# Kernel optimization log

Measured on AMD Instinct MI355X. Metric: run time of the kernel, lower is better.

## Reference

```python
import jax, jax.numpy as jnp
import numpy as np

KS = 5               # kernel_size per spline dimension
K3 = KS ** 3         # 125 weight matrices per SplineConv
NS = [16384, 4096, 1024, 256, 64]  # nodes per hierarchy level
DEG = 8


def spline_basis(pseudo):
    """Degree-1 open B-spline basis for 3D pseudo-coords in [0,1].
    Returns basis [E,8] and weight indices [E,8] into the K3 weights."""
    v = pseudo * (KS - 1)
    bot = jnp.minimum(jnp.floor(v), KS - 2)
    frac = v - bot                                  # [E,3]
    bot = bot.astype(jnp.int32)
    bits = jnp.array([[(s >> d) & 1 for d in range(3)] for s in range(8)], jnp.int32)  # [8,3]
    f = frac[:, None, :]                            # [E,1,3]
    basis = jnp.prod(jnp.where(bits[None] == 1, f, 1.0 - f), axis=-1)   # [E,8]
    strides = jnp.array([1, KS, KS * KS], jnp.int32)
    widx = jnp.sum((bot[:, None, :] + bits[None]) * strides, axis=-1)   # [E,8]
    return basis, widx


def spline_conv(x, src, dst, basis, widx, W, root, bias, n):
    """out_j = (1/deg_j) * sum_{i->j} sum_s B_s(u_ij) x_i W_{k(s)} + x_j root + bias.
    Accumulate basis-weighted source features into per-(node, weight-index)
    buckets, then one dense einsum with the 125 kernel weights."""
    in_c = x.shape[1]
    contrib = basis[..., None] * x[src][:, None, :]          # [E,8,in]
    flat = (dst[:, None] * K3 + widx).reshape(-1)            # [E*8]
    acc = jnp.zeros((n * K3, in_c), x.dtype).at[flat].add(contrib.reshape(-1, in_c))
    out = jnp.einsum('nki,kio->no', acc.reshape(n, K3, in_c), W)
    deg = jnp.zeros((n,), x.dtype).at[dst].add(1.0)
    return out / jnp.maximum(deg, 1.0)[:, None] + x @ root + bias


def setup_inputs() -> dict:
    rng = np.random.default_rng(0)
    inp = {}
    inp['x'] = jnp.asarray(rng.standard_normal((NS[0], 1)), jnp.float32)
    for l in range(4):
        e = NS[l] * DEG
        inp[f'src{l}'] = jnp.asarray(rng.integers(0, NS[l], e), jnp.int32)
        inp[f'dst{l}'] = jnp.asarray(rng.integers(0, NS[l], e), jnp.int32)
        inp[f'pseudo{l}'] = jnp.asarray(rng.random((e, 3)), jnp.float32)
        cl = np.arange(NS[l]) % NS[l + 1]  # guarantees every voxel cluster non-empty
        rng.shuffle(cl)
        inp[f'cluster{l}'] = jnp.asarray(cl, jnp.int32)
    chans = [(1, 32), (32, 32), (32, 64), (64, 64), (64, 64), (64, 64), (64, 64), (64, 64)]
    names = ['1', '12', '2', '3', '4', '5', '6', '7']
    for nm, (ci, co) in zip(names, chans):
        inp[f'W{nm}'] = jnp.asarray(rng.standard_normal((K3, ci, co)) / np.sqrt(8.0 * ci), jnp.float32)
        inp[f'R{nm}'] = jnp.asarray(rng.standard_normal((ci, co)) / np.sqrt(ci), jnp.float32)
        inp[f'B{nm}'] = jnp.zeros((co,), jnp.float32)
    inp['fc1_w'] = jnp.asarray(rng.standard_normal((64, 64)) / 8.0, jnp.float32)
    inp['fc1_b'] = jnp.zeros((64,), jnp.float32)
    inp['fc2_w'] = jnp.asarray(rng.standard_normal((64, 10)) / 8.0, jnp.float32)
    inp['fc2_b'] = jnp.zeros((10,), jnp.float32)
    return inp


def reference(x, pseudo0, pseudo1, pseudo2, pseudo3,
              src0, dst0, src1, dst1, src2, dst2, src3, dst3,
              cluster0, cluster1, cluster2, cluster3,
              W1, R1, B1, W12, R12, B12, W2, R2, B2, W3, R3, B3,
              W4, R4, B4, W5, R5, B5, W6, R6, B6, W7, R7, B7,
              fc1_w, fc1_b, fc2_w, fc2_b):
    elu = jax.nn.elu
    # level 0
    b, wi = spline_basis(pseudo0)
    h = elu(spline_conv(x, src0, dst0, b, wi, W1, R1, B1, NS[0]))
    h = elu(spline_conv(h, src0, dst0, b, wi, W12, R12, B12, NS[0]))
    h = jax.ops.segment_max(h, cluster0, num_segments=NS[1])   # voxel max pool 1
    # level 1
    b, wi = spline_basis(pseudo1)
    h = elu(spline_conv(h, src1, dst1, b, wi, W2, R2, B2, NS[1]))
    h = elu(spline_conv(h, src1, dst1, b, wi, W3, R3, B3, NS[1]))
    h = jax.ops.segment_max(h, cluster1, num_segments=NS[2])   # voxel max pool 2
    # level 2
    b, wi = spline_basis(pseudo2)
    h = elu(spline_conv(h, src2, dst2, b, wi, W4, R4, B4, NS[2]))
    h = elu(spline_conv(h, src2, dst2, b, wi, W5, R5, B5, NS[2]))
    h = jax.ops.segment_max(h, cluster2, num_segments=NS[3])   # voxel max pool 3
    # level 3
    b, wi = spline_basis(pseudo3)
    h = elu(spline_conv(h, src3, dst3, b, wi, W6, R6, B6, NS[3]))
    h = elu(spline_conv(h, src3, dst3, b, wi, W7, R7, B7, NS[3]))
    h = jax.ops.segment_max(h, cluster3, num_segments=NS[4])   # voxel max pool 4
    # readout head (dropout is identity in eval mode)
    g = h.mean(0)[None, :]
    g = g @ fc1_w + fc1_b
    g = g @ fc2_w + fc2_b
    return jax.nn.log_softmax(g, axis=1)
```

## Files before the change

kernel.cpp:

```cpp
#include <hip/hip_runtime.h>
#include <hip/hip_bf16.h>

#define KS 5
#define K3 125

typedef __attribute__((ext_vector_type(8))) short short8;
typedef __attribute__((ext_vector_type(4))) float floatx4;

__device__ inline unsigned enc_f(float f) {
    int b = __float_as_int(f);
    return (b >= 0) ? ((unsigned)b | 0x80000000u) : ~((unsigned)b);
}

__device__ inline unsigned short f2bf(float f) {
    unsigned u = __float_as_uint(f);
    u += 0x7FFFu + ((u >> 16) & 1u);
    return (unsigned short)(u >> 16);
}
__device__ inline float bf2f(unsigned short h) {
    return __uint_as_float((unsigned)h << 16);
}
__device__ inline unsigned pack2bf(float a, float b) {
    return (unsigned)f2bf(a) | ((unsigned)f2bf(b) << 16);
}

__device__ inline void edge_basis(const float* __restrict__ pseudo, int e,
                                  float* bs, int* ks) {
    float fr[3];
    int bot[3];
#pragma unroll
    for (int d = 0; d < 3; ++d) {
        float v = pseudo[e * 3 + d] * (float)(KS - 1);
        float fl = fminf(floorf(v), (float)(KS - 2));
        fr[d] = v - fl;
        bot[d] = (int)fl;
    }
    const int strides[3] = {1, KS, KS * KS};
#pragma unroll
    for (int s = 0; s < 8; ++s) {
        float b = 1.f;
        int w = 0;
#pragma unroll
        for (int d = 0; d < 3; ++d) {
            int bit = (s >> d) & 1;
            b *= bit ? fr[d] : (1.f - fr[d]);
            w += (bot[d] + bit) * strides[d];
        }
        bs[s] = b;
        ks[s] = w;
    }
}

__device__ inline void edge_fracs(const float* __restrict__ pseudo, int e, float* bs) {
    float fr[3];
#pragma unroll
    for (int d = 0; d < 3; ++d) {
        float v = pseudo[e * 3 + d] * (float)(KS - 1);
        float fl = fminf(floorf(v), (float)(KS - 2));
        fr[d] = v - fl;
    }
#pragma unroll
    for (int s = 0; s < 8; ++s) {
        float b = 1.f;
#pragma unroll
        for (int d = 0; d < 3; ++d) b *= ((s >> d) & 1) ? fr[d] : (1.f - fr[d]);
        bs[s] = b;
    }
}

__device__ inline int edge_bucket(const float* __restrict__ pseudo, int e) {
    int kb = 0;
#pragma unroll
    for (int d = 0; d < 3; ++d) {
        float v = pseudo[e * 3 + d] * (float)(KS - 1);
        int fl = (int)fminf(floorf(v), (float)(KS - 2));
        kb += fl << (2 * d);
    }
    return kb;
}

__global__ __launch_bounds__(256) void pre1(
    const float* __restrict__ p0, const float* __restrict__ p1,
    const float* __restrict__ p2, const float* __restrict__ p3,
    const int* __restrict__ d0, const int* __restrict__ d1,
    const int* __restrict__ d2, const int* __restrict__ d3,
    const int* __restrict__ c0, const int* __restrict__ c1,
    const int* __restrict__ c2, const int* __restrict__ c3,
    const float* __restrict__ w12, const float* __restrict__ w2,
    const float* __restrict__ w3, const float* __restrict__ w4,
    const float* __restrict__ w5, const float* __restrict__ w6,
    const float* __restrict__ w7,
    int* __restrict__ hpart, int* __restrict__ degi,
    int* __restrict__ ccnt, int* __restrict__ clist,
    short* __restrict__ Wt, int* __restrict__ posArr) {
    __shared__ float wls[64 * 65];
    __shared__ int h[64];
    int b = blockIdx.x;
    int t = threadIdx.x;
    if (b >= 765) {
        int sl = b - 765;
        const float* srcp;
        int IC, OC, lgI, lgO, per;
        size_t obase;
        if (sl < 125) {
            IC = 32; OC = 32; lgI = 5; lgO = 5; per = 1024;
            srcp = w12 + (size_t)sl * 1024;
            obase = (size_t)sl * 1024;
        } else if (sl < 250) {
            int k = sl - 125;
            IC = 32; OC = 64; lgI = 5; lgO = 6; per = 2048;
            srcp = w2 + (size_t)k * 2048;
            obase = 128000 + (size_t)k * 2048;
        } else {
            int q = sl - 250;
            int ts = q / 125;
            int k = q - ts * 125;
            const float* Ws[5] = {w3, w4, w5, w6, w7};
            IC = 64; OC = 64; lgI = 6; lgO = 6; per = 4096;
            srcp = Ws[ts] + (size_t)k * 4096;
            obase = 384000 + (size_t)ts * 512000 + (size_t)k * 4096;
        }
        for (int r = t; r < per; r += 256) {
            int i = r >> lgO, o = r & (OC - 1);
            wls[i * (OC + 1) + o] = srcp[r];
        }
        __syncthreads();
        for (int j = t; j < per; j += 256) {
            int o = j >> lgI, i = j & (IC - 1);
            Wt[obase + j] = (short)f2bf(wls[i * (OC + 1) + o]);
        }
        return;
    }
    if (b >= 680) {
        int idx = (b - 680) * 256 + t;
        int j, cof, nof;
        const int* cl;
        if (idx < 16384)      { j = idx;         cl = c0; cof = 0;    nof = 0; }
        else if (idx < 20480) { j = idx - 16384; cl = c1; cof = 4096; nof = 16384; }
        else if (idx < 21504) { j = idx - 20480; cl = c2; cof = 5120; nof = 20480; }
        else if (idx < 21760) { j = idx - 21504; cl = c3; cof = 5376; nof = 21504; }
        else return;
        int c = cl[j];
        int slot = atomicAdd(&ccnt[cof + c], 1) & 3;
        clist[nof + c * 4 + slot] = j;
        return;
    }
    int l, lb, E, dof, eof_;
    const float* ps;
    const int* ds;
    if (b < 512)      { l = 0; lb = b;       ps = p0; ds = d0; E = 131072; dof = 0;     eof_ = 0; }
    else if (b < 640) { l = 1; lb = b - 512; ps = p1; ds = d1; E = 32768;  dof = 16384; eof_ = 131072; }
    else if (b < 672) { l = 2; lb = b - 640; ps = p2; ds = d2; E = 8192;   dof = 20480; eof_ = 163840; }
    else              { l = 3; lb = b - 672; ps = p3; ds = d3; E = 2048;   dof = 21504; eof_ = 172032; }
    if (t < 64) h[t] = 0;
    __syncthreads();
    int e = lb * 256 + t;
    if (e < E) {
        atomicAdd(&h[edge_bucket(ps, e)], 1);
        int rel = atomicAdd(&degi[dof + ds[e]], 1);
        posArr[eof_ + e] = rel;
    }
    __syncthreads();
    if (t < 64) hpart[b * 64 + t] = h[t];
}

__global__ __launch_bounds__(1024) void pre2(const int* __restrict__ hpart,
                                             int* __restrict__ bbase,
                                             int* __restrict__ tileOf,
                                             int* __restrict__ pack,
                                             const int* __restrict__ degi,
                                             int* __restrict__ off) {
    int b = blockIdx.x;
    int t = threadIdx.x;
    __shared__ int ls[1024];
    __shared__ int aux[192];
    if (b < 4) {
        const int Nv[4] = {16384, 4096, 1024, 256};
        const int DOFv[4] = {0, 16384, 20480, 21504};
        const int OFFv[4] = {0, 16385, 20482, 21507};
        int l = b;
        int n = Nv[l];
        const int* d = degi + DOFv[l];
        int* o = off + OFFv[l];
        int per = (n + 1023) >> 10;
        int beg = t * per;
        int end = (beg + per < n) ? beg + per : n;
        int s = 0;
        for (int j = beg; j < end; ++j) s += d[j];
        ls[t] = s;
        __syncthreads();
        for (int dd = 1; dd < 1024; dd <<= 1) {
            int v = (t >= dd) ? ls[t - dd] : 0;
            __syncthreads();
            ls[t] += v;
            __syncthreads();
        }
        int base = (t == 0) ? 0 : ls[t - 1];
        for (int j = beg; j < end; ++j) {
            o[j] = base;
            base += d[j];
        }
        if (t == 1023) o[n] = ls[1023];
    } else {
        const int TBv[4] = {0, 2112, 2688, 2880};
        const int MTv[4] = {2112, 576, 192, 96};
        const int HBv[4] = {0, 512, 640, 672};
        const int NBv[4] = {512, 128, 32, 8};
        int l = b - 4;
        int tileBase = TBv[l];
        int hb = HBv[l], nb = NBv[l];
        int bucket = t & 63, seg = t >> 6;
        int rps = (nb + 15) >> 4;
        int r0 = seg * rps;
        int r1 = r0 + rps;
        if (r1 > nb) r1 = nb;
        int ssum = 0;
        for (int lb = r0; lb < r1; ++lb) ssum += hpart[(hb + lb) * 64 + bucket];
        ls[seg * 64 + bucket] = ssum;
        __syncthreads();
        int pre = 0;
        for (int s2 = 0; s2 < seg; ++s2) pre += ls[s2 * 64 + bucket];
        if (seg == 15) aux[bucket] = pre + ssum;
        __syncthreads();
        if (t < 64) aux[64 + t] = (aux[t] + 63) >> 6;
        __syncthreads();
        for (int d = 1; d < 64; d <<= 1) {
            int v = 0;
            if (t < 64 && t >= d) v = aux[64 + t - d];
            __syncthreads();
            if (t < 64) aux[64 + t] += v;
            __syncthreads();
        }
        if (t < 64) {
            int cnt = aux[t];
            int tiles = (cnt + 63) >> 6;
            int tb = tileBase + aux[64 + t] - tiles;
            int gstart = tb * 64;
            aux[128 + t] = gstart;
            for (int q = 0; q < tiles; ++q) tileOf[tb + q] = t;
            for (int idx = gstart + cnt; idx < (tb + tiles) * 64; ++idx) pack[idx] = -1;
            if (t == 63) {
                for (int q = tileBase + aux[64 + 63]; q < tileBase + MTv[l]; ++q)
                    tileOf[q] = -1;
            }
        }
        __syncthreads();
        int run = aux[128 + bucket] + pre;
        for (int lb = r0; lb < r1; ++lb) {
            bbase[(hb + lb) * 64 + bucket] = run;
            run += hpart[(hb + lb) * 64 + bucket];
        }
    }
}

__global__ __launch_bounds__(256) void scatter_pos_all(
    const float* __restrict__ p0, const float* __restrict__ p1,
    const float* __restrict__ p2, const float* __restrict__ p3,
    const int* __restrict__ d0, const int* __restrict__ d1,
    const int* __restrict__ d2, const int* __restrict__ d3,
    const int* __restrict__ bbase, const int* __restrict__ csr,
    int* __restrict__ pack, int* __restrict__ posArr,
    int* __restrict__ esrt) {
    int b = blockIdx.x;
    int l, lb, E, eof_, cof;
    const float* ps;
    const int* ds;
    if (b < 512)      { l = 0; lb = b;       ps = p0; ds = d0; E = 131072; eof_ = 0;      cof = 0; }
    else if (b < 640) { l = 1; lb = b - 512; ps = p1; ds = d1; E = 32768;  eof_ = 131072; cof = 16385; }
    else if (b < 672) { l = 2; lb = b - 640; ps = p2; ds = d2; E = 8192;   eof_ = 163840; cof = 20482; }
    else              { l = 3; lb = b - 672; ps = p3; ds = d3; E = 2048;   eof_ = 172032; cof = 21507; }
    const int* csrL = csr + cof;
    __shared__ int h[64], lbk[64], gb[64], sh[64];
    __shared__ int sp[256];
    __shared__ unsigned char skk[256];
    int t = threadIdx.x;
    int e = lb * 256 + t;
    int kb = -1;
    if (t < 64) {
        h[t] = 0;
        gb[t] = bbase[b * 64 + t];
    }
    __syncthreads();
    if (e < E) {
        kb = edge_bucket(ps, e);
        atomicAdd(&h[kb], 1);
        int p = csrL[ds[e]] + posArr[eof_ + e];
        posArr[eof_ + e] = p;
        if (l == 0 && p >= 0 && p < 131072) esrt[p] = e;
    }
    __syncthreads();
    if (t < 64) sh[t] = h[t];
    __syncthreads();
    for (int d = 1; d < 64; d <<= 1) {
        int v = (t < 64 && t >= d) ? sh[t - d] : 0;
        __syncthreads();
        if (t < 64) sh[t] += v;
        __syncthreads();
    }
    if (t < 64) {
        lbk[t] = sh[t] - h[t];
        h[t] = 0;
    }
    __syncthreads();
    if (kb >= 0) {
        int ppos = lbk[kb] + atomicAdd(&h[kb], 1);
        sp[ppos] = e;
        skk[ppos] = (unsigned char)kb;
    }
    __syncthreads();
    int Pb = E - lb * 256;
    if (Pb > 256) Pb = 256;
    if (t < Pb) {
        int k = skk[t];
        pack[gb[k] + (t - lbk[k])] = sp[t];
    }
}

__global__ __launch_bounds__(256) void conv1_fin(
    const float* __restrict__ x, const int* __restrict__ src,
    const float* __restrict__ pseudo, const int* __restrict__ esrt,
    const int* __restrict__ off, const float* __restrict__ W,
    const float* __restrict__ R, const float* __restrict__ B,
    float* __restrict__ out, int n, int Emax) {
    const int lane = threadIdx.x & 63;
    const int wid = threadIdx.x >> 6;
    const int sub = lane >> 5;
    const int o = lane & 31;
    int j = (blockIdx.x * 4 + wid) * 2 + sub;
    if (j >= n) return;
    int b0 = off[j], b1 = off[j + 1];
    if (b0 < 0) b0 = 0;
    if (b1 > Emax) b1 = Emax;
    float acc = 0.f;
    float px = 0.f, py = 0.f, pz = 0.f, xs = 0.f;
    if (b0 < b1) {
        int e0 = esrt[b0];
        px = pseudo[e0 * 3];
        py = pseudo[e0 * 3 + 1];
        pz = pseudo[e0 * 3 + 2];
        xs = x[src[e0]];
    }
    for (int r = b0; r < b1; ++r) {
        float cpx = px, cpy = py, cpz = pz, cxs = xs;
        if (r + 1 < b1) {
            int e1 = esrt[r + 1];
            px = pseudo[e1 * 3];
            py = pseudo[e1 * 3 + 1];
            pz = pseudo[e1 * 3 + 2];
            xs = x[src[e1]];
        }
        float fr[3];
        int bot[3];
        float pv[3] = {cpx, cpy, cpz};
#pragma unroll
        for (int d = 0; d < 3; ++d) {
            float v = pv[d] * (float)(KS - 1);
            float fl = fminf(floorf(v), (float)(KS - 2));
            fr[d] = v - fl;
            bot[d] = (int)fl;
        }
        const int strides[3] = {1, KS, KS * KS};
        float w = 0.f;
#pragma unroll
        for (int s = 0; s < 8; ++s) {
            float bsv = 1.f;
            int wk = 0;
#pragma unroll
            for (int d = 0; d < 3; ++d) {
                int bit = (s >> d) & 1;
                bsv *= bit ? fr[d] : (1.f - fr[d]);
                wk += (bot[d] + bit) * strides[d];
            }
            w = fmaf(bsv, W[wk * 32 + o], w);
        }
        acc = fmaf(w, cxs, acc);
    }
    float d = fmaxf((float)(b1 - b0), 1.f);
    float v = acc / d + x[j] * R[o] + B[o];
    out[(size_t)j * 32 + o] = (v > 0.f) ? v : expm1f(v);
}

template <int IN_C, int OUT_C>
__global__ __launch_bounds__(256, 6) void mfma_conv(
    const float* __restrict__ x, const int* __restrict__ src,
    const float* __restrict__ pseudo, const int* __restrict__ pack,
    const int* __restrict__ tileOf, const int* __restrict__ pos,
    const short* __restrict__ Wt, unsigned short* __restrict__ y, int tileBase,
    int Emax) {
    constexpr int PH = (IN_C == 64) ? 4 : 2;
    constexpr int SPP = 8 / PH;
    constexpr int KPH = SPP * IN_C;
    constexpr int KP = KPH + 8;
    constexpr int NT = OUT_C / 16;
    constexpr int IP = IN_C / 4;
    __shared__ short As[64 * KP];
    __shared__ int posL[64];
    const int tid = threadIdx.x;
    int t = tileBase + blockIdx.x;
    int kb = tileOf[t];
    if (kb < 0 || kb >= 64) return;
    kb = __builtin_amdgcn_readfirstlane(kb);
    const int kbase = (kb & 3) + 5 * ((kb >> 2) & 3) + 25 * ((kb >> 4) & 3);
    const int eLoc = tid >> 2, part = tid & 3;
    int e = pack[t * 64 + eLoc];
    if (e >= Emax) e = -1;
    float bs[8];
    float4 xq[IP / 4];
    if (e >= 0) edge_fracs(pseudo, e, bs);
    else {
#pragma unroll
        for (int s = 0; s < 8; ++s) bs[s] = 0.f;
    }
    if (part == 0) posL[eLoc] = (e >= 0) ? pos[e] : -1;
#pragma unroll
    for (int g = 0; g < IP / 4; ++g)
        xq[g] = (e >= 0)
                    ? *(const float4*)(x + (size_t)src[e] * IN_C + part * IP + g * 4)
                    : make_float4(0.f, 0.f, 0.f, 0.f);
    const int wave = tid >> 6, lane = tid & 63;
    const int quad = lane >> 4, lm = lane & 15;
    floatx4 acc[NT];
#pragma unroll
    for (int nt = 0; nt < NT; ++nt) acc[nt] = (floatx4){0.f, 0.f, 0.f, 0.f};
    const short* myrow = &As[(wave * 16 + lm) * KP];
#pragma unroll
    for (int ph = 0; ph < PH; ++ph) {
        if (ph) __syncthreads();
#pragma unroll
        for (int s2 = 0; s2 < SPP; ++s2) {
            const float b = bs[ph * SPP + s2];
            short* rowp = &As[eLoc * KP + s2 * IN_C + part * IP];
#pragma unroll
            for (int g = 0; g < IP / 4; ++g) {
                unsigned lo = pack2bf(b * xq[g].x, b * xq[g].y);
                unsigned hi = pack2bf(b * xq[g].z, b * xq[g].w);
                *(uint2*)(rowp + 4 * g) = make_uint2(lo, hi);
            }
        }
        __syncthreads();
#pragma unroll
        for (int kstep = 0; kstep < KPH / 32; ++kstep) {
            const int kg = kstep * 32;
            const int s2 = kg / IN_C;
            const int i0 = kg % IN_C;
            const int s = ph * SPP + s2;
            const int ks = kbase + (s & 1) + 5 * ((s >> 1) & 1) + 25 * ((s >> 2) & 1);
            short8 a = *(const short8*)&myrow[kg + quad * 8];
#pragma unroll
            for (int nt = 0; nt < NT; ++nt) {
                const short* bp =
                    Wt + ((size_t)ks * OUT_C + nt * 16 + lm) * IN_C + i0 + quad * 8;
                short8 bfr = *(const short8*)bp;
                acc[nt] = __builtin_amdgcn_mfma_f32_16x16x32_bf16(a, bfr, acc[nt], 0, 0, 0);
            }
        }
    }
#pragma unroll
    for (int nt = 0; nt < NT; ++nt) {
#pragma unroll
        for (int r = 0; r < 4; ++r) {
            int row = wave * 16 + quad * 4 + r;
            int p = posL[row];
            if (p >= 0 && p < Emax) y[(size_t)p * OUT_C + nt * 16 + lm] = f2bf(acc[nt][r]);
        }
    }
}

template <int OUT_C>
__device__ inline float csr_sum(const int* __restrict__ off,
                                const unsigned short* __restrict__ y, int j, int o,
                                float& dcount) {
    int b0 = off[j], b1 = off[j + 1];
    if (b0 < 0) b0 = 0;
    if (b1 < b0) b1 = b0;
    dcount = fmaxf((float)(b1 - b0), 1.f);
    float s0 = 0.f, s1 = 0.f, s2 = 0.f, s3 = 0.f;
    int r = b0;
    for (; r + 4 <= b1; r += 4) {
        s0 += bf2f(y[(size_t)(r + 0) * OUT_C + o]);
        s1 += bf2f(y[(size_t)(r + 1) * OUT_C + o]);
        s2 += bf2f(y[(size_t)(r + 2) * OUT_C + o]);
        s3 += bf2f(y[(size_t)(r + 3) * OUT_C + o]);
    }
    for (; r < b1; ++r) s0 += bf2f(y[(size_t)r * OUT_C + o]);
    return (s0 + s1) + (s2 + s3);
}

template <int IN_C, int OUT_C>
__global__ __launch_bounds__(256) void fin_gather_k(
    const float* __restrict__ xin, const float* __restrict__ R,
    const float* __restrict__ B, const int* __restrict__ off,
    const unsigned short* __restrict__ y, float* __restrict__ out, int n) {
    const int lane = threadIdx.x & 63;
    const int wid = threadIdx.x >> 6;
    constexpr int EPW = 64 / OUT_C;
    const int sub = (EPW == 2) ? (lane >> 5) : 0;
    const int o = lane & (OUT_C - 1);
    int j = (blockIdx.x * (blockDim.x >> 6) + wid) * EPW + sub;
    if (j >= n) return;
    float xv = (o < IN_C) ? xin[j * IN_C + o] : 0.f;
    float acc = B[o];
#pragma unroll 4
    for (int i = 0; i < IN_C; ++i) {
        float xi = __shfl(xv, i, OUT_C);
        acc = fmaf(xi, R[i * OUT_C + o], acc);
    }
    float d;
    float s = csr_sum<OUT_C>(off, y, j, o, d);
    float v = s / d + acc;
    out[j * OUT_C + o] = (v > 0.f) ? v : expm1f(v);
}

template <int IN_C, int OUT_C>
__global__ __launch_bounds__(256) void fin_pool_k(
    const float* __restrict__ xin, const float* __restrict__ R,
    const float* __restrict__ B, const int* __restrict__ off,
    const unsigned short* __restrict__ y, const int* __restrict__ clist,
    float* __restrict__ out, int nsrc) {
    constexpr int CPB = 256 / (4 * OUT_C);
    const int t = threadIdx.x;
    const int o = t & (OUT_C - 1);
    const int mem = (t / OUT_C) & 3;
    const int g = t / (4 * OUT_C);
    const int c = blockIdx.x * CPB + g;
    int j = clist[c * 4 + mem];
    if (j < 0) j = 0;
    if (j >= nsrc) j = nsrc - 1;
    float xv = (o < IN_C) ? xin[(size_t)j * IN_C + o] : 0.f;
    float acc = B[o];
#pragma unroll 4
    for (int i = 0; i < IN_C; ++i) {
        float xi = __shfl(xv, i, OUT_C);
        acc = fmaf(xi, R[i * OUT_C + o], acc);
    }
    float d;
    float s = csr_sum<OUT_C>(off, y, j, o, d);
    float v = s / d + acc;
    v = (v > 0.f) ? v : expm1f(v);
    __shared__ float sh[256];
    sh[t] = v;
    __syncthreads();
    if (mem == 0) {
        const float* base = &sh[g * 4 * OUT_C];
        float r01 = fmaxf(base[o], base[OUT_C + o]);
        float r23 = fmaxf(base[2 * OUT_C + o], base[3 * OUT_C + o]);
        out[(size_t)c * OUT_C + o] = fmaxf(r01, r23);
    }
}

__global__ __launch_bounds__(256) void conv1_fused(const float* __restrict__ x,
                                                   const int* __restrict__ src,
                                                   const int* __restrict__ dst,
                                                   const float* __restrict__ pseudo,
                                                   const float* __restrict__ W,
                                                   float* __restrict__ out, int E) {
    const int lane = threadIdx.x & 63;
    const int wid = threadIdx.x >> 6;
    const int sub = lane >> 5;
    const int o = lane & 31;
    int e = (blockIdx.x * 4 + wid) * 2 + sub;
    if (e >= E) return;
    float bs[8];
    int ks[8];
    edge_basis(pseudo, e, bs, ks);
    float acc = 0.f;
#pragma unroll
    for (int s = 0; s < 8; ++s) acc = fmaf(bs[s], W[ks[s] * 32 + o], acc);
    atomicAdd(&out[(size_t)dst[e] * 32 + o], acc * x[src[e]]);
}

template <int IN_C, int OUT_C>
__global__ __launch_bounds__(256) void conv_edges_inline(
    const float* __restrict__ x, const int* __restrict__ src,
    const int* __restrict__ dst, const float* __restrict__ pseudo,
    const float* __restrict__ W, float* __restrict__ out, int E) {
    const int lane = threadIdx.x & 63;
    const int wid = threadIdx.x >> 6;
    constexpr int EPW = 64 / OUT_C;
    const int sub = (EPW == 2) ? (lane >> 5) : 0;
    const int o = lane & (OUT_C - 1);
    long e = (long)(blockIdx.x * (blockDim.x >> 6) + wid) * EPW + sub;
    if (e >= E) return;
    float bs[8];
    int ks[8];
    edge_basis(pseudo, e, bs, ks);
    const int s_ = src[e];
    const int d_ = dst[e];
    float xv = (o < IN_C) ? x[s_ * IN_C + o] : 0.f;
    float acc = 0.f;
#pragma unroll
    for (int s = 0; s < 8; ++s) {
        const float b = bs[s];
        const float* Wk = W + (long)ks[s] * IN_C * OUT_C;
#pragma unroll 4
        for (int i = 0; i < IN_C; ++i) {
            float xi = __shfl(xv, i, OUT_C);
            acc = fmaf(b * xi, Wk[i * OUT_C + o], acc);
        }
    }
    atomicAdd(&out[(long)d_ * OUT_C + o], acc);
}

__global__ void deg_kernel(const int* __restrict__ dst, float* __restrict__ deg, int E) {
    int e = blockIdx.x * blockDim.x + threadIdx.x;
    if (e >= E) return;
    atomicAdd(&deg[dst[e]], 1.0f);
}

template <int IN_C, int OUT_C>
__global__ __launch_bounds__(256) void finalize_k(
    const float* __restrict__ xin, const float* __restrict__ R,
    const float* __restrict__ B, const float* __restrict__ deg,
    float* __restrict__ out, int n) {
    const int lane = threadIdx.x & 63;
    const int wid = threadIdx.x >> 6;
    constexpr int EPW = 64 / OUT_C;
    const int sub = (EPW == 2) ? (lane >> 5) : 0;
    const int o = lane & (OUT_C - 1);
    int j = (blockIdx.x * (blockDim.x >> 6) + wid) * EPW + sub;
    if (j >= n) return;
    float xv = (o < IN_C) ? xin[j * IN_C + o] : 0.f;
    float acc = B[o];
#pragma unroll 4
    for (int i = 0; i < IN_C; ++i) {
        float xi = __shfl(xv, i, OUT_C);
        acc = fmaf(xi, R[i * OUT_C + o], acc);
    }
    float d = fmaxf(deg[j], 1.f);
    float v = out[j * OUT_C + o] / d + acc;
    out[j * OUT_C + o] = (v > 0.f) ? v : expm1f(v);
}

__global__ void pool_scatter(const float* __restrict__ h, const int* __restrict__ cluster,
                             unsigned* __restrict__ pool, int n, int logC) {
    int idx = blockIdx.x * blockDim.x + threadIdx.x;
    if (idx >= (n << logC)) return;
    int j = idx >> logC;
    int c = idx & ((1 << logC) - 1);
    atomicMax(&pool[(cluster[j] << logC) + c], enc_f(h[idx]));
}

__global__ void pool_decode(const unsigned* __restrict__ pool, float* __restrict__ out, int total) {
    int idx = blockIdx.x * blockDim.x + threadIdx.x;
    if (idx >= total) return;
    unsigned u = pool[idx];
    int b = (u & 0x80000000u) ? (int)(u & 0x7FFFFFFFu) : (int)(~u);
    out[idx] = __int_as_float(b);
}

__global__ void head_kernel(const float* __restrict__ h, const float* __restrict__ fc1w,
                            const float* __restrict__ fc1b, const float* __restrict__ fc2w,
                            const float* __restrict__ fc2b, float* __restrict__ out) {
    __shared__ float m[64], t[64], u[10];
    int lane = threadIdx.x;
    float s = 0.f;
    for (int j = 0; j < 64; ++j) s += h[j * 64 + lane];
    m[lane] = s * (1.f / 64.f);
    __syncthreads();
    float a = fc1b[lane];
    for (int i = 0; i < 64; ++i) a = fmaf(m[i], fc1w[i * 64 + lane], a);
    t[lane] = a;
    __syncthreads();
    if (lane < 10) {
        float b = fc2b[lane];
        for (int i = 0; i < 64; ++i) b = fmaf(t[i], fc2w[i * 10 + lane], b);
        u[lane] = b;
    }
    __syncthreads();
    if (lane < 10) {
        float mx = u[0];
        for (int i = 1; i < 10; ++i) mx = fmaxf(mx, u[i]);
        float se = 0.f;
        for (int i = 0; i < 10; ++i) se += expf(u[i] - mx);
        out[lane] = u[lane] - mx - logf(se);
    }
}

static inline int cdiv(int a, int b) { return (a + b - 1) / b; }

extern "C" void kernel_launch(void* const* d_in, const int* in_sizes, int n_in,
                              void* d_out, int out_size, void* d_ws, size_t ws_size,
                              hipStream_t stream) {
    const float* x = (const float*)d_in[0];
    const int* src[4] = {(const int*)d_in[1], (const int*)d_in[5], (const int*)d_in[9], (const int*)d_in[13]};
    const int* dst[4] = {(const int*)d_in[2], (const int*)d_in[6], (const int*)d_in[10], (const int*)d_in[14]};
    const float* pseudo[4] = {(const float*)d_in[3], (const float*)d_in[7], (const float*)d_in[11], (const float*)d_in[15]};
    const int* cluster[4] = {(const int*)d_in[4], (const int*)d_in[8], (const int*)d_in[12], (const int*)d_in[16]};
    const float* Wp[8], *Rp[8], *Bp[8];
    for (int l = 0; l < 8; ++l) {
        Wp[l] = (const float*)d_in[17 + 3 * l];
        Rp[l] = (const float*)d_in[18 + 3 * l];
        Bp[l] = (const float*)d_in[19 + 3 * l];
    }
    const float* fc1w = (const float*)d_in[41];
    const float* fc1b = (const float*)d_in[42];
    const float* fc2w = (const float*)d_in[43];
    const float* fc2b = (const float*)d_in[44];
    float* outp = (float*)d_out;

    const int NS[5] = {16384, 4096, 1024, 256, 64};
    const int ES[4] = {16384 * 8, 4096 * 8, 1024 * 8, 256 * 8};
    const int MT[4] = {2048 + 64, 512 + 64, 128 + 64, 32 + 64};
    const int TB_[4] = {0, 2112, 2112 + 576, 2112 + 576 + 192};
    const int TOT_TILES = 2112 + 576 + 192 + 96;
    const int DTOT = 21760;
    const int OFF2[4] = {0, 16385, 20482, 21507};
    const int OFFTOT = 21764;
    const int EBASE[4] = {0, 131072, 163840, 172032};
    const int ETOT = 174080;
    const int NODE_OFF[4] = {0, 16384, 20480, 21504};
    const int CCTOT = 4096 + 1024 + 256 + 64;
    const int HTOT = 680;
    const int WT_OFF[7] = {0, 128000, 384000, 896000, 1408000, 1920000, 2432000};
    const int WT_TOT = 2944000;
    const int NSLICE = 875;

    char* w = (char*)d_ws;
    auto take = [&](size_t bytes) -> char* {
        char* r = w;
        w += (bytes + 255) & ~(size_t)255;
        return r;
    };
    float* bufA = (float*)take((size_t)NS[0] * 64 * 4);
    float* bufB = (float*)take((size_t)NS[0] * 64 * 4);
    unsigned* pool = (unsigned*)take((size_t)NS[1] * 64 * 4);
    char* zbase = w;
    int* ccnt = (int*)take((size_t)CCTOT * 4);
    int* degi = (int*)take((size_t)DTOT * 4);
    size_t zbytes = (size_t)(w - zbase);
    size_t fallbackNeed = (size_t)(w - (char*)d_ws);
    int* tileOf = (int*)take((size_t)TOT_TILES * 4);
    int* hpart = (int*)take((size_t)HTOT * 64 * 4);
    int* bbase = (int*)take((size_t)HTOT * 64 * 4);
    int* pack = (int*)take((size_t)TOT_TILES * 64 * 4);
    int* csr = (int*)take((size_t)OFFTOT * 4);
    int* posArr = (int*)take((size_t)ETOT * 4);
    int* clist = (int*)take((size_t)DTOT * 4);
    int* esrt = (int*)take((size_t)ES[0] * 4);
    short* Wtb = (short*)take((size_t)WT_TOT * 2);
    unsigned short* y = (unsigned short*)take((size_t)ES[0] * 32 * 2);
    size_t need = (size_t)(w - (char*)d_ws);
    bool fast = ws_size >= need;

    const int TB = 256;

    if (fast) {
        (void)hipMemsetAsync(zbase, 0, zbytes, stream);
        pre1<<<765 + NSLICE, 256, 0, stream>>>(
            pseudo[0], pseudo[1], pseudo[2], pseudo[3],
            dst[0], dst[1], dst[2], dst[3],
            cluster[0], cluster[1], cluster[2], cluster[3],
            Wp[1], Wp[2], Wp[3], Wp[4], Wp[5], Wp[6], Wp[7],
            hpart, degi, ccnt, clist, Wtb, posArr);
        pre2<<<8, 1024, 0, stream>>>(hpart, bbase, tileOf, pack, degi, csr);
        scatter_pos_all<<<680, 256, 0, stream>>>(pseudo[0], pseudo[1], pseudo[2], pseudo[3],
                                                 dst[0], dst[1], dst[2], dst[3],
                                                 bbase, csr, pack, posArr, esrt);

        {
            int n = NS[0];
            const int* off = csr + OFF2[0];
            const int* pos = posArr + EBASE[0];
            conv1_fin<<<cdiv(n, 8), TB, 0, stream>>>(x, src[0], pseudo[0], esrt, off,
                                                     Wp[0], Rp[0], Bp[0], bufA, n, ES[0]);
            mfma_conv<32, 32><<<MT[0], TB, 0, stream>>>(
                bufA, src[0], pseudo[0], pack, tileOf, pos, Wtb + WT_OFF[0], y, TB_[0], ES[0]);
            fin_pool_k<32, 32><<<NS[1] / 2, TB, 0, stream>>>(
                bufA, Rp[1], Bp[1], off, y, clist + NODE_OFF[0], bufB, NS[0]);
        }
        {
            int n = NS[1];
            const int* off = csr + OFF2[1];
            const int* pos = posArr + EBASE[1];
            mfma_conv<32, 64><<<MT[1], TB, 0, stream>>>(
                bufB, src[1], pseudo[1], pack, tileOf, pos, Wtb + WT_OFF[1], y, TB_[1], ES[1]);
            fin_gather_k<32, 64><<<cdiv(n, 4), TB, 0, stream>>>(bufB, Rp[2], Bp[2], off, y, bufA, n);
            mfma_conv<64, 64><<<MT[1], TB, 0, stream>>>(
                bufA, src[1], pseudo[1], pack, tileOf, pos, Wtb + WT_OFF[2], y, TB_[1], ES[1]);
            fin_pool_k<64, 64><<<NS[2], TB, 0, stream>>>(
                bufA, Rp[3], Bp[3], off, y, clist + NODE_OFF[1], bufB, NS[1]);
        }
        {
            int n = NS[2];
            const int* off = csr + OFF2[2];
            const int* pos = posArr + EBASE[2];
            mfma_conv<64, 64><<<MT[2], TB, 0, stream>>>(
                bufB, src[2], pseudo[2], pack, tileOf, pos, Wtb + WT_OFF[3], y, TB_[2], ES[2]);
            fin_gather_k<64, 64><<<cdiv(n, 4), TB, 0, stream>>>(bufB, Rp[4], Bp[4], off, y, bufA, n);
            mfma_conv<64, 64><<<MT[2], TB, 0, stream>>>(
                bufA, src[2], pseudo[2], pack, tileOf, pos, Wtb + WT_OFF[4], y, TB_[2], ES[2]);
            fin_pool_k<64, 64><<<NS[3], TB, 0, stream>>>(
                bufA, Rp[5], Bp[5], off, y, clist + NODE_OFF[2], bufB, NS[2]);
        }
        {
            int n = NS[3];
            const int* off = csr + OFF2[3];
            const int* pos = posArr + EBASE[3];
            mfma_conv<64, 64><<<MT[3], TB, 0, stream>>>(
                bufB, src[3], pseudo[3], pack, tileOf, pos, Wtb + WT_OFF[5], y, TB_[3], ES[3]);
            fin_gather_k<64, 64><<<cdiv(n, 4), TB, 0, stream>>>(bufB, Rp[6], Bp[6], off, y, bufA, n);
            mfma_conv<64, 64><<<MT[3], TB, 0, stream>>>(
                bufA, src[3], pseudo[3], pack, tileOf, pos, Wtb + WT_OFF[6], y, TB_[3], ES[3]);
            fin_pool_k<64, 64><<<NS[4], TB, 0, stream>>>(
                bufA, Rp[7], Bp[7], off, y, clist + NODE_OFF[3], bufB, NS[3]);
        }
        head_kernel<<<1, 64, 0, stream>>>(bufB, fc1w, fc1b, fc2w, fc2b, outp);
    } else if (ws_size >= fallbackNeed) {
        float* h0 = bufA;
        float* h1 = bufB;
        float* deg = (float*)degi;
        for (int l = 0; l < 4; ++l) {
            int E = ES[l], n = NS[l];
            (void)hipMemsetAsync(deg, 0, n * 4, stream);
            deg_kernel<<<cdiv(E, TB), TB, 0, stream>>>(dst[l], deg, E);
            for (int cc = 0; cc < 2; ++cc) {
                int li = (l == 0) ? cc : 2 * l + cc;
                if (l == 0 && cc == 0) {
                    (void)hipMemsetAsync(h0, 0, (size_t)n * 32 * 4, stream);
                    conv1_fused<<<cdiv(E, 8), TB, 0, stream>>>(x, src[0], dst[0], pseudo[0], Wp[0], h0, E);
                    finalize_k<1, 32><<<cdiv(n, 8), TB, 0, stream>>>(x, Rp[0], Bp[0], deg, h0, n);
                } else {
                    int ic = (l == 0) ? 32 : ((l == 1 && cc == 0) ? 32 : 64);
                    int oc = (l == 0) ? 32 : 64;
                    (void)hipMemsetAsync(h1, 0, (size_t)n * oc * 4, stream);
                    if (ic == 32 && oc == 32) {
                        conv_edges_inline<32, 32><<<cdiv(E, 8), TB, 0, stream>>>(h0, src[l], dst[l], pseudo[l], Wp[li], h1, E);
                        finalize_k<32, 32><<<cdiv(n, 8), TB, 0, stream>>>(h0, Rp[li], Bp[li], deg, h1, n);
                    } else if (ic == 32) {
                        conv_edges_inline<32, 64><<<cdiv(E, 4), TB, 0, stream>>>(h0, src[l], dst[l], pseudo[l], Wp[li], h1, E);
                        finalize_k<32, 64><<<cdiv(n, 4), TB, 0, stream>>>(h0, Rp[li], Bp[li], deg, h1, n);
                    } else {
                        conv_edges_inline<64, 64><<<cdiv(E, 4), TB, 0, stream>>>(h0, src[l], dst[l], pseudo[l], Wp[li], h1, E);
                        finalize_k<64, 64><<<cdiv(n, 4), TB, 0, stream>>>(h0, Rp[li], Bp[li], deg, h1, n);
                    }
                    float* tmp = h0; h0 = h1; h1 = tmp;
                }
            }
            int oc = (l == 0) ? 32 : 64;
            int logC = (l == 0) ? 5 : 6;
            (void)hipMemsetAsync(pool, 0, (size_t)NS[l + 1] * oc * 4, stream);
            pool_scatter<<<cdiv(n * oc, TB), TB, 0, stream>>>(h0, cluster[l], pool, n, logC);
            pool_decode<<<cdiv(NS[l + 1] * oc, TB), TB, 0, stream>>>(pool, h1, NS[l + 1] * oc);
            float* tmp = h0; h0 = h1; h1 = tmp;
        }
        head_kernel<<<1, 64, 0, stream>>>(h0, fc1w, fc1b, fc2w, fc2b, outp);
    }
}
```

Measured before the change: 388.2 us.

## Process two edge tiles per block with double-buffered LDS in mfma_conv

Each mfma_conv block now handles two consecutive 64-edge tiles. It loads both tiles' edges, basis values and source features up front, then alternates between two LDS buffers so staging one tile can overlap MFMA work on the other. Grid size is halved and the launch bounds occupancy hint drops from 6 to 4 to allow the extra registers and shared memory. The halved grid assumes MT is even (an odd count would drop a tile). Lower occupancy and register pressure from the doubled accumulators may offset the overlap gain.

```diff
diff --git a/kernel.cpp b/kernel.cpp
--- a/kernel.cpp
+++ b/kernel.cpp
@@ -381,7 +381,7 @@
 }
 
 template <int IN_C, int OUT_C>
-__global__ __launch_bounds__(256, 6) void mfma_conv(
+__global__ __launch_bounds__(256, 4) void mfma_conv(
     const float* __restrict__ x, const int* __restrict__ src,
     const float* __restrict__ pseudo, const int* __restrict__ pack,
     const int* __restrict__ tileOf, const int* __restrict__ pos,
@@ -393,75 +393,93 @@
     constexpr int KP = KPH + 8;
     constexpr int NT = OUT_C / 16;
     constexpr int IP = IN_C / 4;
-    __shared__ short As[64 * KP];
-    __shared__ int posL[64];
+    __shared__ short As[2][64 * KP];
+    __shared__ int posL[2][64];
     const int tid = threadIdx.x;
-    int t = tileBase + blockIdx.x;
-    int kb = tileOf[t];
-    if (kb < 0 || kb >= 64) return;
-    kb = __builtin_amdgcn_readfirstlane(kb);
-    const int kbase = (kb & 3) + 5 * ((kb >> 2) & 3) + 25 * ((kb >> 4) & 3);
+    const int t0 = tileBase + 2 * blockIdx.x;
+    int kb0 = tileOf[t0], kb1 = tileOf[t0 + 1];
+    bool v0 = (kb0 >= 0 && kb0 < 64), v1 = (kb1 >= 0 && kb1 < 64);
+    if (!v0 && !v1) return;
+    if (!v0) kb0 = 0;
+    if (!v1) kb1 = 0;
+    kb0 = __builtin_amdgcn_readfirstlane(kb0);
+    kb1 = __builtin_amdgcn_readfirstlane(kb1);
+    const int kbase[2] = {(kb0 & 3) + 5 * ((kb0 >> 2) & 3) + 25 * ((kb0 >> 4) & 3),
+                          (kb1 & 3) + 5 * ((kb1 >> 2) & 3) + 25 * ((kb1 >> 4) & 3)};
     const int eLoc = tid >> 2, part = tid & 3;
-    int e = pack[t * 64 + eLoc];
-    if (e >= Emax) e = -1;
-    float bs[8];
-    float4 xq[IP / 4];
-    if (e >= 0) edge_fracs(pseudo, e, bs);
-    else {
-#pragma unroll
-        for (int s = 0; s < 8; ++s) bs[s] = 0.f;
-    }
-    if (part == 0) posL[eLoc] = (e >= 0) ? pos[e] : -1;
-#pragma unroll
-    for (int g = 0; g < IP / 4; ++g)
-        xq[g] = (e >= 0)
-                    ? *(const float4*)(x + (size_t)src[e] * IN_C + part * IP + g * 4)
-                    : make_float4(0.f, 0.f, 0.f, 0.f);
     const int wave = tid >> 6, lane = tid & 63;
     const int quad = lane >> 4, lm = lane & 15;
-    floatx4 acc[NT];
-#pragma unroll
-    for (int nt = 0; nt < NT; ++nt) acc[nt] = (floatx4){0.f, 0.f, 0.f, 0.f};
-    const short* myrow = &As[(wave * 16 + lm) * KP];
-#pragma unroll
-    for (int ph = 0; ph < PH; ++ph) {
-        if (ph) __syncthreads();
+    int e[2];
+    e[0] = v0 ? pack[(size_t)t0 * 64 + eLoc] : -1;
+    e[1] = v1 ? pack[(size_t)(t0 + 1) * 64 + eLoc] : -1;
+    float bs[2][8];
+    float4 xq[2][IP / 4];
+#pragma unroll
+    for (int q = 0; q < 2; ++q) {
+        if (e[q] >= Emax) e[q] = -1;
+        if (e[q] >= 0) edge_fracs(pseudo, e[q], bs[q]);
+        else {
+#pragma unroll
+            for (int s = 0; s < 8; ++s) bs[q][s] = 0.f;
+        }
+        if (part == 0) posL[q][eLoc] = (e[q] >= 0) ? pos[e[q]] : -1;
+#pragma unroll
+        for (int g = 0; g < IP / 4; ++g)
+            xq[q][g] = (e[q] >= 0)
+                           ? *(const float4*)(x + (size_t)src[e[q]] * IN_C + part * IP + g * 4)
+                           : make_float4(0.f, 0.f, 0.f, 0.f);
+    }
+    floatx4 acc[2][NT];
+#pragma unroll
+    for (int q = 0; q < 2; ++q)
+#pragma unroll
+        for (int nt = 0; nt < NT; ++nt) acc[q][nt] = (floatx4){0.f, 0.f, 0.f, 0.f};
+#pragma unroll
+    for (int p = 0; p < 2 * PH; ++p) {
+        const int q = p & 1;
+        const int ph = p >> 1;
+        short* Ab = As[q];
 #pragma unroll
         for (int s2 = 0; s2 < SPP; ++s2) {
-            const float b = bs[ph * SPP + s2];
-            short* rowp = &As[eLoc * KP + s2 * IN_C + part * IP];
+            const float b = bs[q][ph * SPP + s2];
+            short* rowp = &Ab[eLoc * KP + s2 * IN_C + part * IP];
 #pragma unroll
             for (int g = 0; g < IP / 4; ++g) {
-                unsigned lo = pack2bf(b * xq[g].x, b * xq[g].y);
-                unsigned hi = pack2bf(b * xq[g].z, b * xq[g].w);
+                unsigned lo = pack2bf(b * xq[q][g].x, b * xq[q][g].y);
+                unsigned hi = pack2bf(b * xq[q][g].z, b * xq[q][g].w);
                 *(uint2*)(rowp + 4 * g) = make_uint2(lo, hi);
             }
         }
         __syncthreads();
+        const short* myrow = &Ab[(wave * 16 + lm) * KP];
 #pragma unroll
         for (int kstep = 0; kstep < KPH / 32; ++kstep) {
             const int kg = kstep * 32;
             const int s2 = kg / IN_C;
             const int i0 = kg % IN_C;
             const int s = ph * SPP + s2;
-            const int ks = kbase + (s & 1) + 5 * ((s >> 1) & 1) + 25 * ((s >> 2) & 1);
+            const int ks = kbase[q] + (s & 1) + 5 * ((s >> 1) & 1) + 25 * ((s >> 2) & 1);
             short8 a = *(const short8*)&myrow[kg + quad * 8];
 #pragma unroll
             for (int nt = 0; nt < NT; ++nt) {
                 const short* bp =
                     Wt + ((size_t)ks * OUT_C + nt * 16 + lm) * IN_C + i0 + quad * 8;
                 short8 bfr = *(const short8*)bp;
-                acc[nt] = __builtin_amdgcn_mfma_f32_16x16x32_bf16(a, bfr, acc[nt], 0, 0, 0);
+                acc[q][nt] = __builtin_amdgcn_mfma_f32_16x16x32_bf16(a, bfr, acc[q][nt], 0, 0, 0);
             }
         }
     }
 #pragma unroll
-    for (int nt = 0; nt < NT; ++nt) {
-#pragma unroll
-        for (int r = 0; r < 4; ++r) {
-            int row = wave * 16 + quad * 4 + r;
-            int p = posL[row];
-            if (p >= 0 && p < Emax) y[(size_t)p * OUT_C + nt * 16 + lm] = f2bf(acc[nt][r]);
+    for (int q = 0; q < 2; ++q) {
+#pragma unroll
+        for (int nt = 0; nt < NT; ++nt) {
+#pragma unroll
+            for (int r = 0; r < 4; ++r) {
+                int row = wave * 16 + quad * 4 + r;
+                int p = posL[q][row];
+                if (p >= 0 && p < Emax)
+                    y[(size_t)p * OUT_C + nt * 16 + lm] = f2bf(acc[q][nt][r]);
+            }
         }
     }
 }
@@ -763,7 +781,7 @@
             const int* pos = posArr + EBASE[0];
             conv1_fin<<<cdiv(n, 8), TB, 0, stream>>>(x, src[0], pseudo[0], esrt, off,
                                                      Wp[0], Rp[0], Bp[0], bufA, n, ES[0]);
-            mfma_conv<32, 32><<<MT[0], TB, 0, stream>>>(
+            mfma_conv<32, 32><<<MT[0] / 2, TB, 0, stream>>>(
                 bufA, src[0], pseudo[0], pack, tileOf, pos, Wtb + WT_OFF[0], y, TB_[0], ES[0]);
             fin_pool_k<32, 32><<<NS[1] / 2, TB, 0, stream>>>(
                 bufA, Rp[1], Bp[1], off, y, clist + NODE_OFF[0], bufB, NS[0]);
@@ -772,10 +790,10 @@
             int n = NS[1];
             const int* off = csr + OFF2[1];
             const int* pos = posArr + EBASE[1];
-            mfma_conv<32, 64><<<MT[1], TB, 0, stream>>>(
+            mfma_conv<32, 64><<<MT[1] / 2, TB, 0, stream>>>(
                 bufB, src[1], pseudo[1], pack, tileOf, pos, Wtb + WT_OFF[1], y, TB_[1], ES[1]);
             fin_gather_k<32, 64><<<cdiv(n, 4), TB, 0, stream>>>(bufB, Rp[2], Bp[2], off, y, bufA, n);
-            mfma_conv<64, 64><<<MT[1], TB, 0, stream>>>(
+            mfma_conv<64, 64><<<MT[1] / 2, TB, 0, stream>>>(
                 bufA, src[1], pseudo[1], pack, tileOf, pos, Wtb + WT_OFF[2], y, TB_[1], ES[1]);
             fin_pool_k<64, 64><<<NS[2], TB, 0, stream>>>(
                 bufA, Rp[3], Bp[3], off, y, clist + NODE_OFF[1], bufB, NS[1]);
@@ -784,10 +802,10 @@
             int n = NS[2];
             const int* off = csr + OFF2[2];
             const int* pos = posArr + EBASE[2];
-            mfma_conv<64, 64><<<MT[2], TB, 0, stream>>>(
+            mfma_conv<64, 64><<<MT[2] / 2, TB, 0, stream>>>(
                 bufB, src[2], pseudo[2], pack, tileOf, pos, Wtb + WT_OFF[3], y, TB_[2], ES[2]);
             fin_gather_k<64, 64><<<cdiv(n, 4), TB, 0, stream>>>(bufB, Rp[4], Bp[4], off, y, bufA, n);
-            mfma_conv<64, 64><<<MT[2], TB, 0, stream>>>(
+            mfma_conv<64, 64><<<MT[2] / 2, TB, 0, stream>>>(
                 bufA, src[2], pseudo[2], pack, tileOf, pos, Wtb + WT_OFF[4], y, TB_[2], ES[2]);
             fin_pool_k<64, 64><<<NS[3], TB, 0, stream>>>(
                 bufA, Rp[5], Bp[5], off, y, clist + NODE_OFF[2], bufB, NS[2]);
@@ -796,10 +814,10 @@
             int n = NS[3];
             const int* off = csr + OFF2[3];
             const int* pos = posArr + EBASE[3];
-            mfma_conv<64, 64><<<MT[3], TB, 0, stream>>>(
+            mfma_conv<64, 64><<<MT[3] / 2, TB, 0, stream>>>(
                 bufB, src[3], pseudo[3], pack, tileOf, pos, Wtb + WT_OFF[5], y, TB_[3], ES[3]);
             fin_gather_k<64, 64><<<cdiv(n, 4), TB, 0, stream>>>(bufB, Rp[6], Bp[6], off, y, bufA, n);
-            mfma_conv<64, 64><<<MT[3], TB, 0, stream>>>(
+            mfma_conv<64, 64><<<MT[3] / 2, TB, 0, stream>>>(
                 bufA, src[3], pseudo[3], pack, tileOf, pos, Wtb + WT_OFF[6], y, TB_[3], ES[3]);
             fin_pool_k<64, 64><<<NS[4], TB, 0, stream>>>(
                 bufA, Rp[7], Bp[7], off, y, clist + NODE_OFF[3], bufB, NS[3]);
```

Result: slower. 435.0 us (+12.1%).
